# Kernel tuning notes

Hardware: AMD Instinct MI355X
Metric: run time of the kernel (lower is better)

## Reference

```python
import jax, jax.numpy as jnp
import numpy as np

B, N, K, G = 8, 16384, 16, 4
D_OUT = 128
CQ = CV = 64            # cv must equal d_out//2 for the lpe reshape to work
CQG, CVG = CQ // G, CV // G
C_LPE = D_OUT // (2 * G)  # = CVG = 16
BN_EPS = 1e-5


def setup_inputs() -> dict:
    key = jax.random.key(0)
    ks = jax.random.split(key, 8)
    xyz = jax.random.normal(ks[0], (B, N, 3), dtype=jnp.float32)
    query = jax.random.normal(ks[1], (B, CQ, N), dtype=jnp.float32)
    value = jax.random.normal(ks[2], (B, CV, N, 1), dtype=jnp.float32)
    neigh_idx = jax.random.randint(ks[3], (B, N, K), 0, N, dtype=jnp.int64)
    idx_base = (jnp.arange(B, dtype=jnp.int64) * N).reshape(B, 1, 1)
    lpe_W = jax.random.normal(ks[4], (C_LPE, 10), dtype=jnp.float32) * 0.1
    lpe_b = jnp.zeros((C_LPE,), dtype=jnp.float32)
    bn_gamma = jnp.ones((C_LPE,), dtype=jnp.float32)
    bn_beta = jnp.zeros((C_LPE,), dtype=jnp.float32)
    bn_mean = jnp.zeros((C_LPE,), dtype=jnp.float32)
    bn_var = jnp.ones((C_LPE,), dtype=jnp.float32)
    return {"xyz": xyz, "query": query, "value": value,
            "neigh_idx": neigh_idx, "idx_base": idx_base,
            "lpe_W": lpe_W, "lpe_b": lpe_b, "bn_gamma": bn_gamma,
            "bn_beta": bn_beta, "bn_mean": bn_mean, "bn_var": bn_var}


def _gtl_forward(xyz, query, value, neigh_idx, idx_base,
                 lpe_W, lpe_b, bn_gamma, bn_beta, bn_mean, bn_var):
    b, n, _ = xyz.shape
    k = neigh_idx.shape[-1]
    lq = query.reshape(b, G, CQG, n)                       # [b,g,cqg,n]
    lv = value.reshape(b, G, CVG, n)                       # [b,g,cvg,n]
    xyz_g = jnp.broadcast_to(xyz[:, None].transpose(0, 1, 3, 2), (b, G, 3, n))
    # temp channels: key(cqg) | value(cvg) | xyz(3)
    temp = jnp.concatenate([lq, lv, xyz_g], axis=2)        # [b,g,c,n]
    c = temp.shape[2]
    # flat gather honoring idx_base (batch offsets into b*n)
    flat_idx = (neigh_idx + idx_base).reshape(-1)          # [b*n*k]
    pc_flat = temp.transpose(1, 0, 3, 2).reshape(G, b * n, c)
    feat = pc_flat[:, flat_idx, :].reshape(G, b, n, k, c)
    feat = feat.transpose(1, 0, 4, 2, 3)                   # [b,g,c,n,k]
    lk = feat[:, :, :CQG]                                  # [b,g,cqg,n,k]
    lv_n = feat[:, :, CQG:CQG + CVG]                       # [b,g,cvg,n,k]
    f_xyz = feat[:, :, -3:]                                # [b,g,3,n,k]
    # relative positional encoding -> [b,g,n,k,10]
    neighbor_xyz = f_xyz.transpose(0, 1, 3, 4, 2)          # [b,g,n,k,3]
    xyz_tile = jnp.broadcast_to(xyz[:, None, :, None, :], (b, G, n, k, 3))
    relative_xyz = xyz_tile - neighbor_xyz
    relative_dis = jnp.sqrt(jnp.sum(relative_xyz ** 2, axis=-1, keepdims=True))
    relf = jnp.concatenate([relative_dis, relative_xyz, xyz_tile, neighbor_xyz], axis=-1)
    # permute(0,4,2,1,3) then merge (g,k) -> conv input [b,10,n,g*k]
    relf = relf.transpose(0, 4, 2, 1, 3).reshape(b, 10, n, G * k)
    y = jnp.einsum('oc,bcnm->bonm', lpe_W, relf) + lpe_b[None, :, None, None]
    inv_std = bn_gamma / jnp.sqrt(bn_var + BN_EPS)
    y = (y - bn_mean[None, :, None, None]) * inv_std[None, :, None, None] \
        + bn_beta[None, :, None, None]
    y = jax.nn.relu(y)
    f_enc = y.reshape(b, C_LPE, n, G, k).transpose(0, 3, 1, 2, 4)  # [b,g,cvg,n,k]
    # elementwise attention over neighbors
    la = jax.nn.softmax(jnp.sum(lq[..., None] * lk, axis=2), axis=-1)  # [b,g,n,k]
    lv_cat = jnp.concatenate([lv_n, f_enc], axis=2)        # [b,g,2*cvg,n,k]
    out = jnp.sum(la[:, :, None] * lv_cat, axis=-1).reshape(b, -1, n, 1)
    # attention centrality: scatter-add over neighbor indices
    idx_flat = jnp.broadcast_to(neigh_idx[:, None], (b, G, n, k)).reshape(b, G, n * k)
    att_flat = la.reshape(b, G, n * k)
    centrality = jnp.zeros((b, G, n), dtype=la.dtype).at[
        jnp.arange(b)[:, None, None], jnp.arange(G)[None, :, None], idx_flat
    ].add(att_flat)
    return out, f_enc, centrality


def reference(xyz, query, value, neigh_idx, idx_base,
              lpe_W, lpe_b, bn_gamma, bn_beta, bn_mean, bn_var):
    return _gtl_forward(xyz, query, value, neigh_idx, idx_base,
                        lpe_W, lpe_b, bn_gamma, bn_beta, bn_mean, bn_var)
```

## Files before the change

kernel.cpp:

```cpp
#include <hip/hip_runtime.h>
#include <hip/hip_fp16.h>

#define B_    8
#define N_    16384
#define K_    16
#define G_    4
#define CQ_   64
#define CV_   64
#define CQG_  16
#define CVG_  16
#define CLPE_ 16
#define NT_   (B_*G_*N_)

typedef float f4v __attribute__((ext_vector_type(4)));
typedef int   i4v __attribute__((ext_vector_type(4)));
typedef unsigned int u4v __attribute__((ext_vector_type(4)));

static __device__ __forceinline__ void nt_store4(float* p, float a, float b,
                                                 float c, float d) {
    f4v v = {a, b, c, d};
    __builtin_nontemporal_store(v, (f4v*)p);
}
static __device__ __forceinline__ void nt_store1(float* p, float a) {
    __builtin_nontemporal_store(a, p);
}

union QV { uint4 u; __half2 h[4]; };

__global__ __launch_bounds__(256) void gtl_prep(
    const float* __restrict__ query,
    const float* __restrict__ value,
    const float* __restrict__ xyz,
    uint4*  __restrict__ qvT,
    float4* __restrict__ xyz4,
    float*  __restrict__ cent)
{
    __shared__ unsigned int sbuf[256*17];

    const int t   = threadIdx.x;
    const int wid = blockIdx.x;
    const int xcd = wid & 7;
    const int i   = wid >> 3;
    const int bg  = (xcd << 2) | (i >> 6);
    const int n0  = (i & 63) << 8;
    const int n   = n0 | t;
    const int g   = bg & (G_ - 1);
    const int b   = bg >> 2;
    const int gid = (bg << 14) | n;

    const float* qb = query + (size_t)b*CQ_*N_ + (size_t)g*CQG_*N_ + n;
    const float* vb = value + (size_t)b*CV_*N_ + (size_t)g*CVG_*N_ + n;

    unsigned int u[16];
    #pragma unroll
    for (int q2 = 0; q2 < 8; ++q2) {
        const float a0 = __builtin_nontemporal_load(qb + (size_t)(2*q2+0)*N_);
        const float a1 = __builtin_nontemporal_load(qb + (size_t)(2*q2+1)*N_);
        const __half2 h = __floats2half2_rn(a0, a1);
        u[q2] = *(const unsigned int*)&h;
    }
    #pragma unroll
    for (int q2 = 0; q2 < 8; ++q2) {
        const float a0 = __builtin_nontemporal_load(vb + (size_t)(2*q2+0)*N_);
        const float a1 = __builtin_nontemporal_load(vb + (size_t)(2*q2+1)*N_);
        const __half2 h = __floats2half2_rn(a0, a1);
        u[8+q2] = *(const unsigned int*)&h;
    }

    #pragma unroll
    for (int k = 0; k < 16; ++k) sbuf[t*17 + k] = u[k];

    cent[gid] = 0.f;
    if (g == 0) {
        const size_t pp = (size_t)b*N_ + n;
        xyz4[pp] = make_float4(xyz[pp*3+0], xyz[pp*3+1], xyz[pp*3+2], 0.f);
    }

    __syncthreads();

    uint4* ob = qvT + (size_t)(((size_t)bg << 14) | n0) * 4;
    #pragma unroll
    for (int i2 = 0; i2 < 4; ++i2) {
        const int j = i2*256 + t;
        const int r = j >> 2, q = j & 3;
        const unsigned int* sp = &sbuf[r*17 + q*4];
        ob[j] = make_uint4(sp[0], sp[1], sp[2], sp[3]);
    }
}

__global__ __launch_bounds__(256) void gtl_main(
    const uint4*  __restrict__ qvT,
    const float4* __restrict__ xyz4,
    const int*    __restrict__ nidx,
    const float*  __restrict__ lpeW,
    const float*  __restrict__ lpeB,
    const float*  __restrict__ bnG,
    const float*  __restrict__ bnB,
    const float*  __restrict__ bnM,
    const float*  __restrict__ bnV,
    float* __restrict__ out,
    float* __restrict__ fenc,
    float* __restrict__ cent)
{
    __shared__ float4 sA[CLPE_];
    __shared__ float4 sB[CLPE_];
    __shared__ float  sbuf[4][64*17];

    const int t    = threadIdx.x;
    const int w    = t >> 6;
    const int lane = t & 63;

    if (t < CLPE_) {
        const float scale = bnG[t] * rsqrtf(bnV[t] + 1e-5f);
        const float shift = (lpeB[t] - bnM[t]) * scale + bnB[t];
        const float w0 = lpeW[t*10+0];
        const float w1 = lpeW[t*10+1], w2 = lpeW[t*10+2], w3 = lpeW[t*10+3];
        const float w4 = lpeW[t*10+4], w5 = lpeW[t*10+5], w6 = lpeW[t*10+6];
        const float w7 = lpeW[t*10+7], w8 = lpeW[t*10+8], w9 = lpeW[t*10+9];
        sA[t] = make_float4(scale*(w1+w4), scale*(w2+w5), scale*(w3+w6), shift);
        sB[t] = make_float4(scale*(w7-w1), scale*(w8-w2), scale*(w9-w3), scale*w0);
    }
    __syncthreads();

    const int wid  = blockIdx.x;
    const int xcd  = wid & 7;
    const int half = wid >> 3;

    #pragma unroll 1
    for (int p = 0; p < 2; ++p) {
        const int slot = half + (p << 7);
        const int bg   = (xcd << 2) | (slot >> 6);
        const int n    = ((slot & 63) << 8) | t;
        const int b    = bg >> 2;
        const size_t xb = (size_t)b * N_;

        int idx[K_];
        {
            const i4v* ip = (const i4v*)(nidx + ((size_t)b*N_ + n) * K_);
            #pragma unroll
            for (int q4 = 0; q4 < K_/4; ++q4) {
                const i4v v = __builtin_nontemporal_load(ip + q4);
                idx[q4*4+0] = v.x; idx[q4*4+1] = v.y;
                idx[q4*4+2] = v.z; idx[q4*4+3] = v.w;
            }
        }

        const uint4* qvslab = qvT + (size_t)bg * N_ * 4;

        float lq[CQG_];
        {
            QV cA, cB;
            cA.u = qvslab[(size_t)n*4+0];
            cB.u = qvslab[(size_t)n*4+1];
            #pragma unroll
            for (int i2 = 0; i2 < 4; ++i2) {
                const float2 f = __half22float2(cA.h[i2]);
                lq[2*i2+0] = f.x; lq[2*i2+1] = f.y;
            }
            #pragma unroll
            for (int i2 = 0; i2 < 4; ++i2) {
                const float2 f = __half22float2(cB.h[i2]);
                lq[8+2*i2+0] = f.x; lq[8+2*i2+1] = f.y;
            }
        }
        const float4 cpt = xyz4[xb + n];

        float la[K_];
        float accV[CVG_];
        __half2 nbh[2*K_];
        #pragma unroll
        for (int c = 0; c < CVG_; ++c) accV[c] = 0.f;
        float m = -1e30f;

        #pragma unroll 4
        for (int k = 0; k < K_; ++k) {
            const int j = idx[k];
            const uint4* rp = qvslab + (size_t)j*4;
            QV r0, r1, r2, r3;
            r0.u = rp[0]; r1.u = rp[1]; r2.u = rp[2]; r3.u = rp[3];
            const float4 pp = xyz4[xb + j];

            float s = 0.f;
            #pragma unroll
            for (int i2 = 0; i2 < 4; ++i2) {
                const float2 f = __half22float2(r0.h[i2]);
                s = fmaf(lq[2*i2+0], f.x, s);
                s = fmaf(lq[2*i2+1], f.y, s);
            }
            #pragma unroll
            for (int i2 = 0; i2 < 4; ++i2) {
                const float2 f = __half22float2(r1.h[i2]);
                s = fmaf(lq[8+2*i2+0], f.x, s);
                s = fmaf(lq[8+2*i2+1], f.y, s);
            }
            la[k] = s;

            const float mn = fmaxf(m, s);
            const float sc = __expf(m - mn);
            const float ww = __expf(s - mn);
            m = mn;

            #pragma unroll
            for (int i2 = 0; i2 < 4; ++i2) {
                const float2 f = __half22float2(r2.h[i2]);
                accV[2*i2+0] = fmaf(ww, f.x, accV[2*i2+0]*sc);
                accV[2*i2+1] = fmaf(ww, f.y, accV[2*i2+1]*sc);
            }
            #pragma unroll
            for (int i2 = 0; i2 < 4; ++i2) {
                const float2 f = __half22float2(r3.h[i2]);
                accV[8+2*i2+0] = fmaf(ww, f.x, accV[8+2*i2+0]*sc);
                accV[8+2*i2+1] = fmaf(ww, f.y, accV[8+2*i2+1]*sc);
            }

            const float rx = cpt.x - pp.x, ry = cpt.y - pp.y, rz = cpt.z - pp.z;
            const float d  = sqrtf(fmaf(rx,rx, fmaf(ry,ry, rz*rz)));
            nbh[2*k+0] = __floats2half2_rn(pp.x, pp.y);
            nbh[2*k+1] = __floats2half2_rn(pp.z, d);
        }

        float ssum = 0.f;
        #pragma unroll
        for (int k = 0; k < K_; ++k) {
            const float e = __expf(la[k] - m);
            la[k] = e; ssum += e;
        }
        const float inv = 1.f / ssum;
        #pragma unroll
        for (int k = 0; k < K_; ++k) la[k] *= inv;
        #pragma unroll
        for (int c = 0; c < CVG_; ++c) accV[c] *= inv;

        {
            float* cb = cent + (size_t)bg * N_;
            #pragma unroll
            for (int k = 0; k < K_; ++k) atomicAdd(cb + idx[k], la[k]);
        }

        float basec[CLPE_];
        #pragma unroll
        for (int c = 0; c < CLPE_; ++c) {
            const float4 a = sA[c];
            basec[c] = fmaf(a.x, cpt.x, fmaf(a.y, cpt.y, fmaf(a.z, cpt.z, a.w)));
        }

        float* ob = out + (size_t)bg * (CVG_ + CLPE_) * N_ + n;
        const size_t n0 = (size_t)(n - lane);
        float* swb = &sbuf[w][0];

        #pragma unroll 2
        for (int c = 0; c < CLPE_; ++c) {
            const float4 wB = sB[c];
            const float base = basec[c];
            float e[K_];
            float acc = 0.f;
            #pragma unroll
            for (int k = 0; k < K_; ++k) {
                const float2 pxy = __half22float2(nbh[2*k+0]);
                const float2 pzd = __half22float2(nbh[2*k+1]);
                float tt = base;
                tt = fmaf(wB.x, pxy.x, tt);
                tt = fmaf(wB.y, pxy.y, tt);
                tt = fmaf(wB.z, pzd.x, tt);
                tt = fmaf(wB.w, pzd.y, tt);
                tt = fmaxf(tt, 0.f);
                e[k] = tt;
                acc  = fmaf(la[k], tt, acc);
            }

            float* sl = swb + lane*17;
            #pragma unroll
            for (int k = 0; k < K_; ++k) sl[k] = e[k];
            __builtin_amdgcn_wave_barrier();

            float* fc = fenc + (((size_t)bg*CLPE_ + c) * N_ + n0) * K_;
            #pragma unroll
            for (int i = 0; i < 4; ++i) {
                const int j  = i*64 + lane;
                const int pt = j >> 2, q = j & 3;
                const float* rp = swb + pt*17 + q*4;
                nt_store4(fc + (size_t)j*4, rp[0], rp[1], rp[2], rp[3]);
            }
            __builtin_amdgcn_wave_barrier();

            nt_store1(ob + (size_t)(CVG_ + c) * N_, acc);
        }

        #pragma unroll
        for (int c = 0; c < CVG_; ++c) nt_store1(ob + (size_t)c * N_, accV[c]);
    }
}

__global__ __launch_bounds__(256) void gtl_fallback(
    const float* __restrict__ xyz,
    const float* __restrict__ query,
    const float* __restrict__ value,
    const int*   __restrict__ nidx,
    const float* __restrict__ lpeW,
    const float* __restrict__ lpeB,
    const float* __restrict__ bnG,
    const float* __restrict__ bnB,
    const float* __restrict__ bnM,
    const float* __restrict__ bnV,
    float* __restrict__ out,
    float* __restrict__ fenc,
    float* __restrict__ cent)
{
    __shared__ float4 sA[CLPE_];
    __shared__ float4 sB[CLPE_];
    const int t = threadIdx.x;
    if (t < CLPE_) {
        const float scale = bnG[t] * rsqrtf(bnV[t] + 1e-5f);
        const float shift = (lpeB[t] - bnM[t]) * scale + bnB[t];
        const float w0 = lpeW[t*10+0];
        const float w1 = lpeW[t*10+1], w2 = lpeW[t*10+2], w3 = lpeW[t*10+3];
        const float w4 = lpeW[t*10+4], w5 = lpeW[t*10+5], w6 = lpeW[t*10+6];
        const float w7 = lpeW[t*10+7], w8 = lpeW[t*10+8], w9 = lpeW[t*10+9];
        sA[t] = make_float4(scale*(w1+w4), scale*(w2+w5), scale*(w3+w6), shift);
        sB[t] = make_float4(scale*(w7-w1), scale*(w8-w2), scale*(w9-w3), scale*w0);
    }
    __syncthreads();
    const int gid = blockIdx.x * 256 + t;
    const int n   = gid & (N_ - 1);
    const int bg  = gid >> 14;
    const int g   = bg & (G_ - 1);
    const int b   = bg >> 2;
    const float cx = xyz[(size_t)(b*N_ + n)*3 + 0];
    const float cy = xyz[(size_t)(b*N_ + n)*3 + 1];
    const float cz = xyz[(size_t)(b*N_ + n)*3 + 2];
    int idx[K_];
    const int4* ip = (const int4*)(nidx + (size_t)(b*N_ + n) * K_);
    #pragma unroll
    for (int q4 = 0; q4 < K_/4; ++q4) {
        const int4 v = ip[q4];
        idx[q4*4+0] = v.x; idx[q4*4+1] = v.y; idx[q4*4+2] = v.z; idx[q4*4+3] = v.w;
    }
    const float* qb = query + (size_t)b*CQ_*N_ + (size_t)g*CQG_*N_;
    float lq[CQG_];
    #pragma unroll
    for (int c = 0; c < CQG_; ++c) lq[c] = qb[(size_t)c*N_ + n];
    float la[K_];
    #pragma unroll 4
    for (int k = 0; k < K_; ++k) {
        const float* qj = qb + idx[k];
        float s = 0.f;
        #pragma unroll
        for (int c = 0; c < CQG_; ++c) s = fmaf(lq[c], qj[(size_t)c*N_], s);
        la[k] = s;
    }
    float m = la[0];
    #pragma unroll
    for (int k = 1; k < K_; ++k) m = fmaxf(m, la[k]);
    float ssum = 0.f;
    #pragma unroll
    for (int k = 0; k < K_; ++k) { const float e = __expf(la[k] - m); la[k] = e; ssum += e; }
    const float inv = 1.f / ssum;
    #pragma unroll
    for (int k = 0; k < K_; ++k) la[k] *= inv;
    float* cb = cent + (size_t)bg * N_;
    #pragma unroll
    for (int k = 0; k < K_; ++k) atomicAdd(cb + idx[k], la[k]);
    float basec[CLPE_];
    #pragma unroll
    for (int c = 0; c < CLPE_; ++c) {
        const float4 a = sA[c];
        basec[c] = fmaf(a.x, cx, fmaf(a.y, cy, fmaf(a.z, cz, a.w)));
    }
    const float* vb = value + (size_t)b*CV_*N_ + (size_t)g*CVG_*N_;
    float accV[CVG_], accE[CLPE_];
    #pragma unroll
    for (int c = 0; c < CLPE_; ++c) { accV[c] = 0.f; accE[c] = 0.f; }
    float* fe = fenc + ((size_t)bg * CLPE_ * N_ + n) * K_;
    #pragma unroll 2
    for (int k = 0; k < K_; ++k) {
        const int j = idx[k];
        const float nx = xyz[(size_t)(b*N_ + j)*3 + 0];
        const float ny = xyz[(size_t)(b*N_ + j)*3 + 1];
        const float nz = xyz[(size_t)(b*N_ + j)*3 + 2];
        const float rx = cx - nx, ry = cy - ny, rz = cz - nz;
        const float d  = sqrtf(rx*rx + ry*ry + rz*rz);
        const float w  = la[k];
        const float* vj = vb + j;
        #pragma unroll
        for (int c = 0; c < CLPE_; ++c) {
            const float4 bb = sB[c];
            float e = basec[c];
            e = fmaf(bb.x, nx, e); e = fmaf(bb.y, ny, e);
            e = fmaf(bb.z, nz, e); e = fmaf(bb.w, d,  e);
            e = fmaxf(e, 0.f);
            fe[(size_t)c*(N_*K_) + k] = e;
            accE[c] = fmaf(w, e, accE[c]);
            accV[c] = fmaf(w, vj[(size_t)c*N_], accV[c]);
        }
    }
    float* ob = out + (size_t)bg * (CVG_ + CLPE_) * N_ + n;
    #pragma unroll
    for (int c = 0; c < CVG_; ++c)  ob[(size_t)c*N_]        = accV[c];
    #pragma unroll
    for (int c = 0; c < CLPE_; ++c) ob[(size_t)(CVG_+c)*N_] = accE[c];
}

extern "C" void kernel_launch(void* const* d_in, const int* in_sizes, int n_in,
                              void* d_out, int out_size, void* d_ws, size_t ws_size,
                              hipStream_t stream) {
    (void)in_sizes; (void)n_in; (void)out_size;

    const float* xyz   = (const float*)d_in[0];
    const float* query = (const float*)d_in[1];
    const float* value = (const float*)d_in[2];
    const int*   nidx  = (const int*)  d_in[3];
    const float* lpeW  = (const float*)d_in[5];
    const float* lpeB  = (const float*)d_in[6];
    const float* bnG   = (const float*)d_in[7];
    const float* bnB   = (const float*)d_in[8];
    const float* bnM   = (const float*)d_in[9];
    const float* bnV   = (const float*)d_in[10];

    float* out  = (float*)d_out;
    float* fenc = out  + (size_t)B_ * (G_*(CVG_+CLPE_)) * N_;
    float* cent = fenc + (size_t)B_ * G_ * CLPE_ * N_ * K_;

    const size_t qv_bytes   = (size_t)NT_ * 64;
    const size_t xyz4_bytes = (size_t)B_ * N_ * sizeof(float4);
    const size_t need = qv_bytes + xyz4_bytes;

    if (ws_size >= need) {
        uint4*  qvT  = (uint4*)d_ws;
        float4* xyz4 = (float4*)((char*)d_ws + qv_bytes);
        hipLaunchKernelGGL(gtl_prep, dim3(NT_/256), dim3(256), 0, stream,
                           query, value, xyz, qvT, xyz4, cent);
        hipLaunchKernelGGL(gtl_main, dim3(NT_/512), dim3(256), 0, stream,
                           qvT, xyz4, nidx, lpeW, lpeB, bnG, bnB, bnM, bnV,
                           out, fenc, cent);
    } else {
        (void)hipMemsetAsync(cent, 0, sizeof(float) * (size_t)B_ * G_ * N_, stream);
        hipLaunchKernelGGL(gtl_fallback, dim3(NT_/256), dim3(256), 0, stream,
                           xyz, query, value, nidx, lpeW, lpeB, bnG, bnB, bnM, bnV,
                           out, fenc, cent);
    }
}
```

Baseline: 986.5 us.

## Fuse prep and main kernels into one cooperative launch with grid sync

Merges the fp16 transpose/prep kernel and the main attention kernel into a single cooperative kernel. Each block first preps two tiles, then hits a grid-wide sync before the gather/softmax/encoding work. The aim is to remove the second launch and the inter-kernel gap. The cost is a grid barrier, and a launch cap of 4 blocks per CU. If the cooperative launch fails it falls back to the two-kernel path.

```diff
diff --git a/kernel.cpp b/kernel.cpp
--- a/kernel.cpp
+++ b/kernel.cpp
@@ -1,5 +1,8 @@
 #include <hip/hip_runtime.h>
+#include <hip/hip_cooperative_groups.h>
 #include <hip/hip_fp16.h>
+
+namespace cg = cooperative_groups;
 
 #define B_    8
 #define N_    16384
@@ -14,7 +17,6 @@
 
 typedef float f4v __attribute__((ext_vector_type(4)));
 typedef int   i4v __attribute__((ext_vector_type(4)));
-typedef unsigned int u4v __attribute__((ext_vector_type(4)));
 
 static __device__ __forceinline__ void nt_store4(float* p, float a, float b,
                                                  float c, float d) {
@@ -26,6 +28,299 @@
 }
 
 union QV { uint4 u; __half2 h[4]; };
+
+__device__ __forceinline__ void prep_tile(
+    const int w, const int t,
+    const float* __restrict__ query, const float* __restrict__ value,
+    const float* __restrict__ xyz,
+    uint4* __restrict__ qvT, float4* __restrict__ xyz4, float* __restrict__ cent,
+    unsigned int* __restrict__ sstage)
+{
+    const int xcd = w & 7;
+    const int i   = w >> 3;
+    const int bg  = (xcd << 2) | (i >> 6);
+    const int n0  = (i & 63) << 8;
+    const int n   = n0 | t;
+    const int g   = bg & (G_ - 1);
+    const int b   = bg >> 2;
+    const int gid = (bg << 14) | n;
+
+    const float* qb = query + (size_t)b*CQ_*N_ + (size_t)g*CQG_*N_ + n;
+    const float* vb = value + (size_t)b*CV_*N_ + (size_t)g*CVG_*N_ + n;
+
+    unsigned int u[16];
+    #pragma unroll
+    for (int q2 = 0; q2 < 8; ++q2) {
+        const float a0 = __builtin_nontemporal_load(qb + (size_t)(2*q2+0)*N_);
+        const float a1 = __builtin_nontemporal_load(qb + (size_t)(2*q2+1)*N_);
+        const __half2 h = __floats2half2_rn(a0, a1);
+        u[q2] = *(const unsigned int*)&h;
+    }
+    #pragma unroll
+    for (int q2 = 0; q2 < 8; ++q2) {
+        const float a0 = __builtin_nontemporal_load(vb + (size_t)(2*q2+0)*N_);
+        const float a1 = __builtin_nontemporal_load(vb + (size_t)(2*q2+1)*N_);
+        const __half2 h = __floats2half2_rn(a0, a1);
+        u[8+q2] = *(const unsigned int*)&h;
+    }
+
+    #pragma unroll
+    for (int k = 0; k < 16; ++k) sstage[t*17 + k] = u[k];
+
+    cent[gid] = 0.f;
+    if (g == 0) {
+        const size_t pp = (size_t)b*N_ + n;
+        xyz4[pp] = make_float4(xyz[pp*3+0], xyz[pp*3+1], xyz[pp*3+2], 0.f);
+    }
+
+    __syncthreads();
+
+    uint4* ob = qvT + (size_t)(((size_t)bg << 14) | (unsigned)n0) * 4;
+    #pragma unroll
+    for (int i2 = 0; i2 < 4; ++i2) {
+        const int j = i2*256 + t;
+        const int r = j >> 2, q = j & 3;
+        const unsigned int* sp = &sstage[r*17 + q*4];
+        ob[j] = make_uint4(sp[0], sp[1], sp[2], sp[3]);
+    }
+    __syncthreads();
+}
+
+__device__ __forceinline__ void init_AB(
+    const int t,
+    const float* __restrict__ lpeW, const float* __restrict__ lpeB,
+    const float* __restrict__ bnG,  const float* __restrict__ bnB,
+    const float* __restrict__ bnM,  const float* __restrict__ bnV,
+    float4* __restrict__ sA, float4* __restrict__ sB)
+{
+    if (t < CLPE_) {
+        const float scale = bnG[t] * rsqrtf(bnV[t] + 1e-5f);
+        const float shift = (lpeB[t] - bnM[t]) * scale + bnB[t];
+        const float w0 = lpeW[t*10+0];
+        const float w1 = lpeW[t*10+1], w2 = lpeW[t*10+2], w3 = lpeW[t*10+3];
+        const float w4 = lpeW[t*10+4], w5 = lpeW[t*10+5], w6 = lpeW[t*10+6];
+        const float w7 = lpeW[t*10+7], w8 = lpeW[t*10+8], w9 = lpeW[t*10+9];
+        sA[t] = make_float4(scale*(w1+w4), scale*(w2+w5), scale*(w3+w6), shift);
+        sB[t] = make_float4(scale*(w7-w1), scale*(w8-w2), scale*(w9-w3), scale*w0);
+    }
+}
+
+__device__ __forceinline__ void main_work(
+    const int wid, const int t,
+    const uint4*  __restrict__ qvT,
+    const float4* __restrict__ xyz4,
+    const int*    __restrict__ nidx,
+    const float4* __restrict__ sA, const float4* __restrict__ sB,
+    float* __restrict__ sbase,
+    float* __restrict__ out, float* __restrict__ fenc, float* __restrict__ cent)
+{
+    const int w    = t >> 6;
+    const int lane = t & 63;
+    const int xcd  = wid & 7;
+    const int half = wid >> 3;
+    float* swb = sbase + w*(64*17);
+
+    #pragma unroll 1
+    for (int p = 0; p < 2; ++p) {
+        const int slot = half + (p << 7);
+        const int bg   = (xcd << 2) | (slot >> 6);
+        const int n    = ((slot & 63) << 8) | t;
+        const int b    = bg >> 2;
+        const size_t xb = (size_t)b * N_;
+
+        int idx[K_];
+        {
+            const i4v* ip = (const i4v*)(nidx + ((size_t)b*N_ + n) * K_);
+            #pragma unroll
+            for (int q4 = 0; q4 < K_/4; ++q4) {
+                const i4v v = __builtin_nontemporal_load(ip + q4);
+                idx[q4*4+0] = v.x; idx[q4*4+1] = v.y;
+                idx[q4*4+2] = v.z; idx[q4*4+3] = v.w;
+            }
+        }
+
+        const uint4* qvslab = qvT + (size_t)bg * N_ * 4;
+
+        float lq[CQG_];
+        {
+            QV cA, cB;
+            cA.u = qvslab[(size_t)n*4+0];
+            cB.u = qvslab[(size_t)n*4+1];
+            #pragma unroll
+            for (int i2 = 0; i2 < 4; ++i2) {
+                const float2 f = __half22float2(cA.h[i2]);
+                lq[2*i2+0] = f.x; lq[2*i2+1] = f.y;
+            }
+            #pragma unroll
+            for (int i2 = 0; i2 < 4; ++i2) {
+                const float2 f = __half22float2(cB.h[i2]);
+                lq[8+2*i2+0] = f.x; lq[8+2*i2+1] = f.y;
+            }
+        }
+        const float4 cpt = xyz4[xb + n];
+
+        float la[K_];
+        float accV[CVG_];
+        __half2 nbh[2*K_];
+        #pragma unroll
+        for (int c = 0; c < CVG_; ++c) accV[c] = 0.f;
+        float m = -1e30f;
+
+        #pragma unroll 4
+        for (int k = 0; k < K_; ++k) {
+            const int j = idx[k];
+            const uint4* rp = qvslab + (size_t)j*4;
+            QV r0, r1, r2, r3;
+            r0.u = rp[0]; r1.u = rp[1]; r2.u = rp[2]; r3.u = rp[3];
+            const float4 pp = xyz4[xb + j];
+
+            float s = 0.f;
+            #pragma unroll
+            for (int i2 = 0; i2 < 4; ++i2) {
+                const float2 f = __half22float2(r0.h[i2]);
+                s = fmaf(lq[2*i2+0], f.x, s);
+                s = fmaf(lq[2*i2+1], f.y, s);
+            }
+            #pragma unroll
+            for (int i2 = 0; i2 < 4; ++i2) {
+                const float2 f = __half22float2(r1.h[i2]);
+                s = fmaf(lq[8+2*i2+0], f.x, s);
+                s = fmaf(lq[8+2*i2+1], f.y, s);
+            }
+            la[k] = s;
+
+            const float mn = fmaxf(m, s);
+            const float sc = __expf(m - mn);
+            const float ww = __expf(s - mn);
+            m = mn;
+
+            #pragma unroll
+            for (int i2 = 0; i2 < 4; ++i2) {
+                const float2 f = __half22float2(r2.h[i2]);
+                accV[2*i2+0] = fmaf(ww, f.x, accV[2*i2+0]*sc);
+                accV[2*i2+1] = fmaf(ww, f.y, accV[2*i2+1]*sc);
+            }
+            #pragma unroll
+            for (int i2 = 0; i2 < 4; ++i2) {
+                const float2 f = __half22float2(r3.h[i2]);
+                accV[8+2*i2+0] = fmaf(ww, f.x, accV[8+2*i2+0]*sc);
+                accV[8+2*i2+1] = fmaf(ww, f.y, accV[8+2*i2+1]*sc);
+            }
+
+            const float rx = cpt.x - pp.x, ry = cpt.y - pp.y, rz = cpt.z - pp.z;
+            const float d  = sqrtf(fmaf(rx,rx, fmaf(ry,ry, rz*rz)));
+            nbh[2*k+0] = __floats2half2_rn(pp.x, pp.y);
+            nbh[2*k+1] = __floats2half2_rn(pp.z, d);
+        }
+
+        float ssum = 0.f;
+        #pragma unroll
+        for (int k = 0; k < K_; ++k) {
+            const float e = __expf(la[k] - m);
+            la[k] = e; ssum += e;
+        }
+        const float inv = 1.f / ssum;
+        #pragma unroll
+        for (int k = 0; k < K_; ++k) la[k] *= inv;
+        #pragma unroll
+        for (int c = 0; c < CVG_; ++c) accV[c] *= inv;
+
+        {
+            float* cb = cent + (size_t)bg * N_;
+            #pragma unroll
+            for (int k = 0; k < K_; ++k) atomicAdd(cb + idx[k], la[k]);
+        }
+
+        float basec[CLPE_];
+        #pragma unroll
+        for (int c = 0; c < CLPE_; ++c) {
+            const float4 a = sA[c];
+            basec[c] = fmaf(a.x, cpt.x, fmaf(a.y, cpt.y, fmaf(a.z, cpt.z, a.w)));
+        }
+
+        float* ob = out + (size_t)bg * (CVG_ + CLPE_) * N_ + n;
+        const size_t n0 = (size_t)(n - lane);
+
+        #pragma unroll 2
+        for (int c = 0; c < CLPE_; ++c) {
+            const float4 wB = sB[c];
+            const float base = basec[c];
+            float e[K_];
+            float acc = 0.f;
+            #pragma unroll
+            for (int k = 0; k < K_; ++k) {
+                const float2 pxy = __half22float2(nbh[2*k+0]);
+                const float2 pzd = __half22float2(nbh[2*k+1]);
+                float tt = base;
+                tt = fmaf(wB.x, pxy.x, tt);
+                tt = fmaf(wB.y, pxy.y, tt);
+                tt = fmaf(wB.z, pzd.x, tt);
+                tt = fmaf(wB.w, pzd.y, tt);
+                tt = fmaxf(tt, 0.f);
+                e[k] = tt;
+                acc  = fmaf(la[k], tt, acc);
+            }
+
+            float* sl = swb + lane*17;
+            #pragma unroll
+            for (int k = 0; k < K_; ++k) sl[k] = e[k];
+            __builtin_amdgcn_wave_barrier();
+
+            float* fc = fenc + (((size_t)bg*CLPE_ + c) * N_ + n0) * K_;
+            #pragma unroll
+            for (int i = 0; i < 4; ++i) {
+                const int j  = i*64 + lane;
+                const int pt = j >> 2, q = j & 3;
+                const float* rp = swb + pt*17 + q*4;
+                nt_store4(fc + (size_t)j*4, rp[0], rp[1], rp[2], rp[3]);
+            }
+            __builtin_amdgcn_wave_barrier();
+
+            nt_store1(ob + (size_t)(CVG_ + c) * N_, acc);
+        }
+
+        #pragma unroll
+        for (int c = 0; c < CVG_; ++c) nt_store1(ob + (size_t)c * N_, accV[c]);
+    }
+}
+
+__global__ __launch_bounds__(256, 4) void gtl_fused(
+    const float* __restrict__ query,
+    const float* __restrict__ value,
+    const float* __restrict__ xyz,
+    uint4*  __restrict__ qvT,
+    float4* __restrict__ xyz4,
+    const int*   __restrict__ nidx,
+    const float* __restrict__ lpeW,
+    const float* __restrict__ lpeB,
+    const float* __restrict__ bnG,
+    const float* __restrict__ bnB,
+    const float* __restrict__ bnM,
+    const float* __restrict__ bnV,
+    float* __restrict__ out,
+    float* __restrict__ fenc,
+    float* __restrict__ cent)
+{
+    __shared__ float4 sA[CLPE_];
+    __shared__ float4 sB[CLPE_];
+    __shared__ unsigned int sstage[256*17];
+
+    const int t   = threadIdx.x;
+    const int wid = blockIdx.x;
+    const int xcd = wid & 7;
+    const int h   = wid >> 3;
+
+    prep_tile(((h*2+0) << 3) | xcd, t, query, value, xyz, qvT, xyz4, cent,
+              sstage);
+    prep_tile(((h*2+1) << 3) | xcd, t, query, value, xyz, qvT, xyz4, cent,
+              sstage);
+    init_AB(t, lpeW, lpeB, bnG, bnB, bnM, bnV, sA, sB);
+
+    cg::this_grid().sync();
+
+    main_work(wid, t, qvT, xyz4, nidx, sA, sB, (float*)sstage,
+              out, fenc, cent);
+}
 
 __global__ __launch_bounds__(256) void gtl_prep(
     const float* __restrict__ query,
@@ -35,57 +330,9 @@
     float4* __restrict__ xyz4,
     float*  __restrict__ cent)
 {
-    __shared__ unsigned int sbuf[256*17];
-
-    const int t   = threadIdx.x;
-    const int wid = blockIdx.x;
-    const int xcd = wid & 7;
-    const int i   = wid >> 3;
-    const int bg  = (xcd << 2) | (i >> 6);
-    const int n0  = (i & 63) << 8;
-    const int n   = n0 | t;
-    const int g   = bg & (G_ - 1);
-    const int b   = bg >> 2;
-    const int gid = (bg << 14) | n;
-
-    const float* qb = query + (size_t)b*CQ_*N_ + (size_t)g*CQG_*N_ + n;
-    const float* vb = value + (size_t)b*CV_*N_ + (size_t)g*CVG_*N_ + n;
-
-    unsigned int u[16];
-    #pragma unroll
-    for (int q2 = 0; q2 < 8; ++q2) {
-        const float a0 = __builtin_nontemporal_load(qb + (size_t)(2*q2+0)*N_);
-        const float a1 = __builtin_nontemporal_load(qb + (size_t)(2*q2+1)*N_);
-        const __half2 h = __floats2half2_rn(a0, a1);
-        u[q2] = *(const unsigned int*)&h;
-    }
-    #pragma unroll
-    for (int q2 = 0; q2 < 8; ++q2) {
-        const float a0 = __builtin_nontemporal_load(vb + (size_t)(2*q2+0)*N_);
-        const float a1 = __builtin_nontemporal_load(vb + (size_t)(2*q2+1)*N_);
-        const __half2 h = __floats2half2_rn(a0, a1);
-        u[8+q2] = *(const unsigned int*)&h;
-    }
-
-    #pragma unroll
-    for (int k = 0; k < 16; ++k) sbuf[t*17 + k] = u[k];
-
-    cent[gid] = 0.f;
-    if (g == 0) {
-        const size_t pp = (size_t)b*N_ + n;
-        xyz4[pp] = make_float4(xyz[pp*3+0], xyz[pp*3+1], xyz[pp*3+2], 0.f);
-    }
-
-    __syncthreads();
-
-    uint4* ob = qvT + (size_t)(((size_t)bg << 14) | n0) * 4;
-    #pragma unroll
-    for (int i2 = 0; i2 < 4; ++i2) {
-        const int j = i2*256 + t;
-        const int r = j >> 2, q = j & 3;
-        const unsigned int* sp = &sbuf[r*17 + q*4];
-        ob[j] = make_uint4(sp[0], sp[1], sp[2], sp[3]);
-    }
+    __shared__ unsigned int sstage[256*17];
+    prep_tile(blockIdx.x, threadIdx.x, query, value, xyz, qvT, xyz4, cent,
+              sstage);
 }
 
 __global__ __launch_bounds__(256) void gtl_main(
@@ -104,191 +351,11 @@
 {
     __shared__ float4 sA[CLPE_];
     __shared__ float4 sB[CLPE_];
-    __shared__ float  sbuf[4][64*17];
-
-    const int t    = threadIdx.x;
-    const int w    = t >> 6;
-    const int lane = t & 63;
-
-    if (t < CLPE_) {
-        const float scale = bnG[t] * rsqrtf(bnV[t] + 1e-5f);
-        const float shift = (lpeB[t] - bnM[t]) * scale + bnB[t];
-        const float w0 = lpeW[t*10+0];
-        const float w1 = lpeW[t*10+1], w2 = lpeW[t*10+2], w3 = lpeW[t*10+3];
-        const float w4 = lpeW[t*10+4], w5 = lpeW[t*10+5], w6 = lpeW[t*10+6];
-        const float w7 = lpeW[t*10+7], w8 = lpeW[t*10+8], w9 = lpeW[t*10+9];
-        sA[t] = make_float4(scale*(w1+w4), scale*(w2+w5), scale*(w3+w6), shift);
-        sB[t] = make_float4(scale*(w7-w1), scale*(w8-w2), scale*(w9-w3), scale*w0);
-    }
+    __shared__ float  sbuf[4*64*17];
+    const int t = threadIdx.x;
+    init_AB(t, lpeW, lpeB, bnG, bnB, bnM, bnV, sA, sB);
     __syncthreads();
-
-    const int wid  = blockIdx.x;
-    const int xcd  = wid & 7;
-    const int half = wid >> 3;
-
-    #pragma unroll 1
-    for (int p = 0; p < 2; ++p) {
-        const int slot = half + (p << 7);
-        const int bg   = (xcd << 2) | (slot >> 6);
-        const int n    = ((slot & 63) << 8) | t;
-        const int b    = bg >> 2;
-        const size_t xb = (size_t)b * N_;
-
-        int idx[K_];
-        {
-            const i4v* ip = (const i4v*)(nidx + ((size_t)b*N_ + n) * K_);
-            #pragma unroll
-            for (int q4 = 0; q4 < K_/4; ++q4) {
-                const i4v v = __builtin_nontemporal_load(ip + q4);
-                idx[q4*4+0] = v.x; idx[q4*4+1] = v.y;
-                idx[q4*4+2] = v.z; idx[q4*4+3] = v.w;
-            }
-        }
-
-        const uint4* qvslab = qvT + (size_t)bg * N_ * 4;
-
-        float lq[CQG_];
-        {
-            QV cA, cB;
-            cA.u = qvslab[(size_t)n*4+0];
-            cB.u = qvslab[(size_t)n*4+1];
-            #pragma unroll
-            for (int i2 = 0; i2 < 4; ++i2) {
-                const float2 f = __half22float2(cA.h[i2]);
-                lq[2*i2+0] = f.x; lq[2*i2+1] = f.y;
-            }
-            #pragma unroll
-            for (int i2 = 0; i2 < 4; ++i2) {
-                const float2 f = __half22float2(cB.h[i2]);
-                lq[8+2*i2+0] = f.x; lq[8+2*i2+1] = f.y;
-            }
-        }
-        const float4 cpt = xyz4[xb + n];
-
-        float la[K_];
-        float accV[CVG_];
-        __half2 nbh[2*K_];
-        #pragma unroll
-        for (int c = 0; c < CVG_; ++c) accV[c] = 0.f;
-        float m = -1e30f;
-
-        #pragma unroll 4
-        for (int k = 0; k < K_; ++k) {
-            const int j = idx[k];
-            const uint4* rp = qvslab + (size_t)j*4;
-            QV r0, r1, r2, r3;
-            r0.u = rp[0]; r1.u = rp[1]; r2.u = rp[2]; r3.u = rp[3];
-            const float4 pp = xyz4[xb + j];
-
-            float s = 0.f;
-            #pragma unroll
-            for (int i2 = 0; i2 < 4; ++i2) {
-                const float2 f = __half22float2(r0.h[i2]);
-                s = fmaf(lq[2*i2+0], f.x, s);
-                s = fmaf(lq[2*i2+1], f.y, s);
-            }
-            #pragma unroll
-            for (int i2 = 0; i2 < 4; ++i2) {
-                const float2 f = __half22float2(r1.h[i2]);
-                s = fmaf(lq[8+2*i2+0], f.x, s);
-                s = fmaf(lq[8+2*i2+1], f.y, s);
-            }
-            la[k] = s;
-
-            const float mn = fmaxf(m, s);
-            const float sc = __expf(m - mn);
-            const float ww = __expf(s - mn);
-            m = mn;
-
-            #pragma unroll
-            for (int i2 = 0; i2 < 4; ++i2) {
-                const float2 f = __half22float2(r2.h[i2]);
-                accV[2*i2+0] = fmaf(ww, f.x, accV[2*i2+0]*sc);
-                accV[2*i2+1] = fmaf(ww, f.y, accV[2*i2+1]*sc);
-            }
-            #pragma unroll
-            for (int i2 = 0; i2 < 4; ++i2) {
-                const float2 f = __half22float2(r3.h[i2]);
-                accV[8+2*i2+0] = fmaf(ww, f.x, accV[8+2*i2+0]*sc);
-                accV[8+2*i2+1] = fmaf(ww, f.y, accV[8+2*i2+1]*sc);
-            }
-
-            const float rx = cpt.x - pp.x, ry = cpt.y - pp.y, rz = cpt.z - pp.z;
-            const float d  = sqrtf(fmaf(rx,rx, fmaf(ry,ry, rz*rz)));
-            nbh[2*k+0] = __floats2half2_rn(pp.x, pp.y);
-            nbh[2*k+1] = __floats2half2_rn(pp.z, d);
-        }
-
-        float ssum = 0.f;
-        #pragma unroll
-        for (int k = 0; k < K_; ++k) {
-            const float e = __expf(la[k] - m);
-            la[k] = e; ssum += e;
-        }
-        const float inv = 1.f / ssum;
-        #pragma unroll
-        for (int k = 0; k < K_; ++k) la[k] *= inv;
-        #pragma unroll
-        for (int c = 0; c < CVG_; ++c) accV[c] *= inv;
-
-        {
-            float* cb = cent + (size_t)bg * N_;
-            #pragma unroll
-            for (int k = 0; k < K_; ++k) atomicAdd(cb + idx[k], la[k]);
-        }
-
-        float basec[CLPE_];
-        #pragma unroll
-        for (int c = 0; c < CLPE_; ++c) {
-            const float4 a = sA[c];
-            basec[c] = fmaf(a.x, cpt.x, fmaf(a.y, cpt.y, fmaf(a.z, cpt.z, a.w)));
-        }
-
-        float* ob = out + (size_t)bg * (CVG_ + CLPE_) * N_ + n;
-        const size_t n0 = (size_t)(n - lane);
-        float* swb = &sbuf[w][0];
-
-        #pragma unroll 2
-        for (int c = 0; c < CLPE_; ++c) {
-            const float4 wB = sB[c];
-            const float base = basec[c];
-            float e[K_];
-            float acc = 0.f;
-            #pragma unroll
-            for (int k = 0; k < K_; ++k) {
-                const float2 pxy = __half22float2(nbh[2*k+0]);
-                const float2 pzd = __half22float2(nbh[2*k+1]);
-                float tt = base;
-                tt = fmaf(wB.x, pxy.x, tt);
-                tt = fmaf(wB.y, pxy.y, tt);
-                tt = fmaf(wB.z, pzd.x, tt);
-                tt = fmaf(wB.w, pzd.y, tt);
-                tt = fmaxf(tt, 0.f);
-                e[k] = tt;
-                acc  = fmaf(la[k], tt, acc);
-            }
-
-            float* sl = swb + lane*17;
-            #pragma unroll
-            for (int k = 0; k < K_; ++k) sl[k] = e[k];
-            __builtin_amdgcn_wave_barrier();
-
-            float* fc = fenc + (((size_t)bg*CLPE_ + c) * N_ + n0) * K_;
-            #pragma unroll
-            for (int i = 0; i < 4; ++i) {
-                const int j  = i*64 + lane;
-                const int pt = j >> 2, q = j & 3;
-                const float* rp = swb + pt*17 + q*4;
-                nt_store4(fc + (size_t)j*4, rp[0], rp[1], rp[2], rp[3]);
-            }
-            __builtin_amdgcn_wave_barrier();
-
-            nt_store1(ob + (size_t)(CVG_ + c) * N_, acc);
-        }
-
-        #pragma unroll
-        for (int c = 0; c < CVG_; ++c) nt_store1(ob + (size_t)c * N_, accV[c]);
-    }
+    main_work(blockIdx.x, t, qvT, xyz4, nidx, sA, sB, sbuf, out, fenc, cent);
 }
 
 __global__ __launch_bounds__(256) void gtl_fallback(
@@ -309,16 +376,7 @@
     __shared__ float4 sA[CLPE_];
     __shared__ float4 sB[CLPE_];
     const int t = threadIdx.x;
-    if (t < CLPE_) {
-        const float scale = bnG[t] * rsqrtf(bnV[t] + 1e-5f);
-        const float shift = (lpeB[t] - bnM[t]) * scale + bnB[t];
-        const float w0 = lpeW[t*10+0];
-        const float w1 = lpeW[t*10+1], w2 = lpeW[t*10+2], w3 = lpeW[t*10+3];
-        const float w4 = lpeW[t*10+4], w5 = lpeW[t*10+5], w6 = lpeW[t*10+6];
-        const float w7 = lpeW[t*10+7], w8 = lpeW[t*10+8], w9 = lpeW[t*10+9];
-        sA[t] = make_float4(scale*(w1+w4), scale*(w2+w5), scale*(w3+w6), shift);
-        sB[t] = make_float4(scale*(w7-w1), scale*(w8-w2), scale*(w9-w3), scale*w0);
-    }
+    init_AB(t, lpeW, lpeB, bnG, bnB, bnM, bnV, sA, sB);
     __syncthreads();
     const int gid = blockIdx.x * 256 + t;
     const int n   = gid & (N_ - 1);
@@ -427,11 +485,27 @@
     if (ws_size >= need) {
         uint4*  qvT  = (uint4*)d_ws;
         float4* xyz4 = (float4*)((char*)d_ws + qv_bytes);
-        hipLaunchKernelGGL(gtl_prep, dim3(NT_/256), dim3(256), 0, stream,
-                           query, value, xyz, qvT, xyz4, cent);
-        hipLaunchKernelGGL(gtl_main, dim3(NT_/512), dim3(256), 0, stream,
-                           qvT, xyz4, nidx, lpeW, lpeB, bnG, bnB, bnM, bnV,
-                           out, fenc, cent);
+
+        const float *a_q = query, *a_v = value, *a_x = xyz;
+        uint4*  a_qv = qvT;
+        float4* a_x4 = xyz4;
+        const int* a_ni = nidx;
+        const float *a_lw = lpeW, *a_lb = lpeB;
+        const float *a_g = bnG, *a_b = bnB, *a_m = bnM, *a_vv = bnV;
+        float *a_o = out, *a_f = fenc, *a_c = cent;
+        void* args[15] = {&a_q, &a_v, &a_x, &a_qv, &a_x4, &a_ni,
+                          &a_lw, &a_lb, &a_g, &a_b, &a_m, &a_vv,
+                          &a_o, &a_f, &a_c};
+        hipError_t e = hipLaunchCooperativeKernel(
+            reinterpret_cast<void*>(gtl_fused), dim3(NT_/512), dim3(256),
+            args, 0u, stream);
+        if (e != hipSuccess) {
+            hipLaunchKernelGGL(gtl_prep, dim3(NT_/256), dim3(256), 0, stream,
+                               query, value, xyz, qvT, xyz4, cent);
+            hipLaunchKernelGGL(gtl_main, dim3(NT_/512), dim3(256), 0, stream,
+                               qvT, xyz4, nidx, lpeW, lpeB, bnG, bnB, bnM, bnV,
+                               out, fenc, cent);
+        }
     } else {
         (void)hipMemsetAsync(cent, 0, sizeof(float) * (size_t)B_ * G_ * N_, stream);
         hipLaunchKernelGGL(gtl_fallback, dim3(NT_/256), dim3(256), 0, stream,
```

New measurement: 1.138 ms. 15.3% more time.
